# Kernel optimization log

Hardware: AMD Instinct MI355X
Metric: run time of the kernel (lower is better)

The kernel has to match this reference:

```python
import jax, jax.numpy as jnp
import numpy as np

EMBED_DIM = 1024
NUM_HEADS = 16
HEAD_DIM = EMBED_DIM // NUM_HEADS
B, T = 4, 2048


def quantum_layer(x):
    # Exact closed form of the RY + CNOT-chain + PauliZ circuit:
    # expval(Z_i) = prod_{j<=i} cos(x_j)  (cumulative product along feature dim)
    return jnp.cumprod(jnp.cos(x), axis=-1)


def separate_heads(x):
    b, s, _ = x.shape
    return x.reshape(b, s, NUM_HEADS, HEAD_DIM).transpose(0, 2, 1, 3)  # (B,H,T,D)


def combine_heads(x):
    b, h, s, d = x.shape
    return x.transpose(0, 2, 1, 3).reshape(b, s, h * d)


def setup_inputs() -> dict:
    key = jax.random.key(0)
    ks = jax.random.split(key, 9)
    scale = 1.0 / np.sqrt(EMBED_DIM)
    return {
        "x": jax.random.normal(ks[0], (B, T, EMBED_DIM), dtype=jnp.float32),
        "Wq": jax.random.normal(ks[1], (EMBED_DIM, EMBED_DIM), dtype=jnp.float32) * scale,
        "bq": jax.random.normal(ks[2], (EMBED_DIM,), dtype=jnp.float32) * 0.01,
        "Wk": jax.random.normal(ks[3], (EMBED_DIM, EMBED_DIM), dtype=jnp.float32) * scale,
        "bk": jax.random.normal(ks[4], (EMBED_DIM,), dtype=jnp.float32) * 0.01,
        "Wv": jax.random.normal(ks[5], (EMBED_DIM, EMBED_DIM), dtype=jnp.float32) * scale,
        "bv": jax.random.normal(ks[6], (EMBED_DIM,), dtype=jnp.float32) * 0.01,
        "Wo": jax.random.normal(ks[7], (EMBED_DIM, EMBED_DIM), dtype=jnp.float32) * scale,
        "bo": jax.random.normal(ks[8], (EMBED_DIM,), dtype=jnp.float32) * 0.01,
    }


def reference(x, Wq, bq, Wk, bk, Wv, bv, Wo, bo):
    k = x @ Wk + bk
    q = x @ Wq + bq
    v = x @ Wv + bv
    # quantum circuit applied to q and k projections
    q = quantum_layer(q)
    k = quantum_layer(k)
    # NOTE: source swaps roles: kqv = (heads(k), heads(q), heads(v)); q, h, v = kqv
    qh = separate_heads(k)   # acts as query
    kh = separate_heads(q)   # acts as key
    vh = separate_heads(v)
    scores = jnp.einsum("bhqd,bhkd->bhqk", qh, kh) / jnp.sqrt(jnp.float32(HEAD_DIM))
    attn = jax.nn.softmax(scores, axis=-1)  # dropout is identity in eval
    out = jnp.einsum("bhqk,bhkd->bhqd", attn, vh)
    return combine_heads(out) @ Wo + bo
```

## Files before the change

kernel.cpp:

```cpp
#include <hip/hip_runtime.h>
#include <hip/hip_bf16.h>

#define B_ 4
#define T_ 2048
#define E_ 1024
#define H_ 16
#define D_ 64
#define M_ (B_ * T_)

typedef unsigned short u16;
typedef unsigned int u32;
typedef short s16x8 __attribute__((ext_vector_type(8)));
typedef unsigned short u16x8 __attribute__((ext_vector_type(8)));
typedef float f32x4 __attribute__((ext_vector_type(4)));
typedef unsigned int u32x2 __attribute__((ext_vector_type(2)));

__device__ __forceinline__ u16 f2bf(float f) {
    __hip_bfloat16 h = __float2bfloat16(f);
    return __builtin_bit_cast(u16, h);
}
__device__ __forceinline__ float bf2f(u16 u) {
    unsigned int v = ((unsigned int)u) << 16;
    return __builtin_bit_cast(float, v);
}
__device__ __forceinline__ u32 pk2(float a, float b) {
    return (u32)f2bf(a) | ((u32)f2bf(b) << 16);
}

__device__ __forceinline__ int block_probe_is_bf16(const void* x, int tid) {
    const u16* p = (const u16*)x;
    u16 u = p[tid];
    int e = (u >> 7) & 0xFF;
    int ok = ((u & 0x7FFF) == 0 || (e >= 103 && e <= 133)) ? 1 : 0;
    return (__syncthreads_count(ok) >= 240) ? 1 : 0;
}

__global__ __launch_bounds__(256) void transpose_w_single_kernel(
    const void* __restrict__ w0, const void* __restrict__ w1,
    u16* __restrict__ o0, u16* __restrict__ o1,
    const void* __restrict__ xprobe)
{
    __shared__ u16 th[64][66];
    const int x = threadIdx.x, y = threadIdx.y;
    const int isbf = block_probe_is_bf16(xprobe, y * 64 + x);
    const void* in = blockIdx.z ? w1 : w0;
    u16* o = blockIdx.z ? o1 : o0;
    const int r0 = blockIdx.y * 64;
    const int c0 = blockIdx.x * 64;
    #pragma unroll
    for (int j = 0; j < 16; j++) {
        const size_t idx = (size_t)(r0 + y * 16 + j) * E_ + c0 + x;
        float v = isbf ? bf2f(((const u16*)in)[idx]) : ((const float*)in)[idx];
        th[y * 16 + j][x] = f2bf(v);
    }
    __syncthreads();
    #pragma unroll
    for (int j = 0; j < 16; j++)
        o[(size_t)(c0 + y * 16 + j) * E_ + r0 + x] = th[x][y * 16 + j];
}

__global__ __launch_bounds__(256) void convert_bias_kernel(
    const void* __restrict__ bq, const void* __restrict__ bk,
    const void* __restrict__ bv, const void* __restrict__ bo,
    float* __restrict__ outb, const void* __restrict__ xprobe)
{
    const int isbf = block_probe_is_bf16(xprobe, threadIdx.x);
    const int i = blockIdx.x * 256 + threadIdx.x;
    const int w = blockIdx.y;
    const void* p = (w == 0) ? bq : (w == 1) ? bk : (w == 2) ? bv : bo;
    float v = isbf ? bf2f(((const u16*)p)[i]) : ((const float*)p)[i];
    outb[w * 1024 + i] = v;
}

__global__ __launch_bounds__(256) void gemm_f32out_kernel(
    const void* __restrict__ A, int a_mode, int m_base,
    const u16* __restrict__ Bt, const float* __restrict__ bias,
    float* __restrict__ Cout, int ldc)
{
    __shared__ u16 a_lds[128 * 72];
    __shared__ u16 b_lds[128 * 72];
    const int tid = threadIdx.x;
    const int isbf = block_probe_is_bf16(A, tid);
    const int a_bf = (a_mode < 0) ? isbf : a_mode;
    const int wave = tid >> 6, lane = tid & 63;
    const int lane15 = lane & 15, quad = lane >> 4;
    const int wm = (wave & 1) * 64, wn = (wave >> 1) * 64;
    const int nwg = (int)(gridDim.x * gridDim.y);
    const int lin = (int)(blockIdx.y * gridDim.x + blockIdx.x);
    const int swz = (lin & 7) * (nwg >> 3) + (lin >> 3);
    const int m0 = (swz / (int)gridDim.x) * 128;
    const int n0 = (swz % (int)gridDim.x) * 128;
    const int srow = tid >> 1;
    const int soff = (tid & 1) * 32;

    f32x4 acc[4][4];
    #pragma unroll
    for (int i = 0; i < 4; i++)
        #pragma unroll
        for (int j = 0; j < 4; j++) acc[i][j] = (f32x4)0.0f;

    const u16* abase_bf = (const u16*)A + (size_t)(m_base + m0 + srow) * E_ + soff;
    const float* abase_f = (const float*)A + (size_t)(m_base + m0 + srow) * E_ + soff;
    const u16* bbase = Bt + (size_t)(n0 + srow) * E_ + soff;

    u16x8 av[4], bv[4];
    if (a_bf) {
        #pragma unroll
        for (int j = 0; j < 4; j++) av[j] = *(const u16x8*)(abase_bf + j * 8);
    } else {
        #pragma unroll
        for (int j = 0; j < 4; j++) {
            f32x4 t0 = *(const f32x4*)(abase_f + j * 8);
            f32x4 t1 = *(const f32x4*)(abase_f + j * 8 + 4);
            u16x8 o;
            #pragma unroll
            for (int e = 0; e < 4; e++) { o[e] = f2bf(t0[e]); o[4 + e] = f2bf(t1[e]); }
            av[j] = o;
        }
    }
    #pragma unroll
    for (int j = 0; j < 4; j++) bv[j] = *(const u16x8*)(bbase + j * 8);

    for (int kk = 0; kk < E_; kk += 64) {
        __syncthreads();
        #pragma unroll
        for (int j = 0; j < 4; j++) {
            *(u16x8*)&a_lds[srow * 72 + soff + j * 8] = av[j];
            *(u16x8*)&b_lds[srow * 72 + soff + j * 8] = bv[j];
        }
        __syncthreads();
        if (kk + 64 < E_) {
            const int k2 = kk + 64;
            if (a_bf) {
                #pragma unroll
                for (int j = 0; j < 4; j++) av[j] = *(const u16x8*)(abase_bf + k2 + j * 8);
            } else {
                #pragma unroll
                for (int j = 0; j < 4; j++) {
                    f32x4 t0 = *(const f32x4*)(abase_f + k2 + j * 8);
                    f32x4 t1 = *(const f32x4*)(abase_f + k2 + j * 8 + 4);
                    u16x8 o;
                    #pragma unroll
                    for (int e = 0; e < 4; e++) { o[e] = f2bf(t0[e]); o[4 + e] = f2bf(t1[e]); }
                    av[j] = o;
                }
            }
            #pragma unroll
            for (int j = 0; j < 4; j++) bv[j] = *(const u16x8*)(bbase + k2 + j * 8);
        }
        #pragma unroll
        for (int ks = 0; ks < 2; ks++) {
            s16x8 af[4], bfr[4];
            #pragma unroll
            for (int i = 0; i < 4; i++)
                af[i] = *(const s16x8*)&a_lds[(wm + i * 16 + lane15) * 72 + ks * 32 + quad * 8];
            #pragma unroll
            for (int j = 0; j < 4; j++)
                bfr[j] = *(const s16x8*)&b_lds[(wn + j * 16 + lane15) * 72 + ks * 32 + quad * 8];
            #pragma unroll
            for (int i = 0; i < 4; i++)
                #pragma unroll
                for (int j = 0; j < 4; j++)
                    acc[i][j] = __builtin_amdgcn_mfma_f32_16x16x32_bf16(af[i], bfr[j], acc[i][j], 0, 0, 0);
        }
    }

    #pragma unroll
    for (int j = 0; j < 4; j++) {
        const int col = n0 + wn + j * 16 + lane15;
        const float bb = bias[col];
        #pragma unroll
        for (int i = 0; i < 4; i++) {
            const int row = m0 + wm + i * 16 + quad * 4;
            #pragma unroll
            for (int r = 0; r < 4; r++)
                Cout[(size_t)(row + r) * ldc + col] = acc[i][j][r] + bb;
        }
    }
}

__global__ __launch_bounds__(256) void gemm_v_fused_kernel(
    const void* __restrict__ X, const u16* __restrict__ Bt,
    const float* __restrict__ bias, u16* __restrict__ Vt)
{
    __shared__ u16 smem[2 * 128 * 72];
    u16* a_lds = smem;
    u16* b_lds = smem + 128 * 72;
    const int tid = threadIdx.x;
    const int isbf = block_probe_is_bf16(X, tid);
    const int wave = tid >> 6, lane = tid & 63;
    const int lane15 = lane & 15, quad = lane >> 4;
    const int wm = (wave & 1) * 64, wn = (wave >> 1) * 64;
    const int nwg = (int)(gridDim.x * gridDim.y);
    const int lin = (int)(blockIdx.y * gridDim.x + blockIdx.x);
    const int swz = (lin & 7) * (nwg >> 3) + (lin >> 3);
    const int m0 = (swz / (int)gridDim.x) * 128;
    const int n0 = (swz % (int)gridDim.x) * 128;
    const int srow = tid >> 1;
    const int soff = (tid & 1) * 32;

    f32x4 acc[4][4];
    #pragma unroll
    for (int i = 0; i < 4; i++)
        #pragma unroll
        for (int j = 0; j < 4; j++) acc[i][j] = (f32x4)0.0f;

    const u16* abase_bf = (const u16*)X + (size_t)(m0 + srow) * E_ + soff;
    const float* abase_f = (const float*)X + (size_t)(m0 + srow) * E_ + soff;
    const u16* bbase = Bt + (size_t)(n0 + srow) * E_ + soff;

    u16x8 av[4], bv[4];
    if (isbf) {
        #pragma unroll
        for (int j = 0; j < 4; j++) av[j] = *(const u16x8*)(abase_bf + j * 8);
    } else {
        #pragma unroll
        for (int j = 0; j < 4; j++) {
            f32x4 t0 = *(const f32x4*)(abase_f + j * 8);
            f32x4 t1 = *(const f32x4*)(abase_f + j * 8 + 4);
            u16x8 o;
            #pragma unroll
            for (int e = 0; e < 4; e++) { o[e] = f2bf(t0[e]); o[4 + e] = f2bf(t1[e]); }
            av[j] = o;
        }
    }
    #pragma unroll
    for (int j = 0; j < 4; j++) bv[j] = *(const u16x8*)(bbase + j * 8);

    for (int kk = 0; kk < E_; kk += 64) {
        __syncthreads();
        #pragma unroll
        for (int j = 0; j < 4; j++) {
            *(u16x8*)&a_lds[srow * 72 + soff + j * 8] = av[j];
            *(u16x8*)&b_lds[srow * 72 + soff + j * 8] = bv[j];
        }
        __syncthreads();
        if (kk + 64 < E_) {
            const int k2 = kk + 64;
            if (isbf) {
                #pragma unroll
                for (int j = 0; j < 4; j++) av[j] = *(const u16x8*)(abase_bf + k2 + j * 8);
            } else {
                #pragma unroll
                for (int j = 0; j < 4; j++) {
                    f32x4 t0 = *(const f32x4*)(abase_f + k2 + j * 8);
                    f32x4 t1 = *(const f32x4*)(abase_f + k2 + j * 8 + 4);
                    u16x8 o;
                    #pragma unroll
                    for (int e = 0; e < 4; e++) { o[e] = f2bf(t0[e]); o[4 + e] = f2bf(t1[e]); }
                    av[j] = o;
                }
            }
            #pragma unroll
            for (int j = 0; j < 4; j++) bv[j] = *(const u16x8*)(bbase + k2 + j * 8);
        }
        #pragma unroll
        for (int ks = 0; ks < 2; ks++) {
            s16x8 af[4], bfr[4];
            #pragma unroll
            for (int i = 0; i < 4; i++)
                af[i] = *(const s16x8*)&a_lds[(wm + i * 16 + lane15) * 72 + ks * 32 + quad * 8];
            #pragma unroll
            for (int j = 0; j < 4; j++)
                bfr[j] = *(const s16x8*)&b_lds[(wn + j * 16 + lane15) * 72 + ks * 32 + quad * 8];
            #pragma unroll
            for (int i = 0; i < 4; i++)
                #pragma unroll
                for (int j = 0; j < 4; j++)
                    acc[i][j] = __builtin_amdgcn_mfma_f32_16x16x32_bf16(af[i], bfr[j], acc[i][j], 0, 0, 0);
        }
    }

    __syncthreads();
    u16* c_tile = smem;
    #pragma unroll
    for (int j = 0; j < 4; j++) {
        const float bb = bias[n0 + wn + j * 16 + lane15];
        #pragma unroll
        for (int i = 0; i < 4; i++)
            #pragma unroll
            for (int r = 0; r < 4; r++)
                c_tile[(wm + i * 16 + quad * 4 + r) * 132 + wn + j * 16 + lane15] =
                    f2bf(acc[i][j][r] + bb);
    }
    __syncthreads();
    const int b = m0 >> 11, t0 = m0 & 2047;
    const int orow = tid >> 1, half = tid & 1;
    u16* dst = Vt + ((size_t)b * 1024 + n0 + orow) * T_ + t0 + half * 64;
    #pragma unroll
    for (int c = 0; c < 8; c++) {
        u16x8 o;
        #pragma unroll
        for (int e = 0; e < 8; e++)
            o[e] = c_tile[(half * 64 + c * 8 + e) * 132 + orow];
        *(u16x8*)(dst + c * 8) = o;
    }
}

__global__ __launch_bounds__(256) void quantum2_kernel(
    const float* __restrict__ in, u16* __restrict__ key, u16* __restrict__ qry)
{
    const int wave = threadIdx.x >> 6, lane = threadIdx.x & 63;
    const int unit = (int)blockIdx.x * 4 + wave;
    const int row = unit >> 1, seg = unit & 1;
    const float* p = in + (size_t)row * 2048 + seg * 1024 + lane * 16;
    float v[16];
    #pragma unroll
    for (int j = 0; j < 16; j += 4) {
        f32x4 t = *(const f32x4*)(p + j);
        v[j] = t[0]; v[j + 1] = t[1]; v[j + 2] = t[2]; v[j + 3] = t[3];
    }
    float pl[16];
    float run = 1.0f;
    #pragma unroll
    for (int j = 0; j < 16; j++) { run *= cosf(v[j]); pl[j] = run; }
    float incl = run;
    #pragma unroll
    for (int off = 1; off < 64; off <<= 1) {
        float t = __shfl_up(incl, off);
        if (lane >= off) incl *= t;
    }
    float pref = __shfl_up(incl, 1);
    if (lane == 0) pref = 1.0f;
    u16x8 o0, o1;
    #pragma unroll
    for (int j = 0; j < 8; j++) {
        o0[j] = f2bf(pref * pl[j]);
        o1[j] = f2bf(pref * pl[j + 8]);
    }
    u16* outp = (seg ? qry : key) + (size_t)row * E_ + lane * 16;
    *(u16x8*)(outp) = o0;
    *(u16x8*)(outp + 8) = o1;
}

__global__ __launch_bounds__(256, 4) void attn_kernel(
    const u16* __restrict__ Qrm, const u16* __restrict__ Krm,
    const u16* __restrict__ Vt, u16* __restrict__ Orm)
{
    __shared__ u16 k_lds[64 * 72];
    __shared__ u16 v_lds[64 * 72];
    __shared__ u16 p_lds[128 * 72];
    const int tid = threadIdx.x;
    const int wave = tid >> 6, lane = tid & 63;
    const int lane15 = lane & 15, quad = lane >> 4;

    const int lin = (int)(blockIdx.x + gridDim.x * blockIdx.y);
    const int swz = (lin & 7) * 128 + (lin >> 3);
    const int t0 = (swz & 15) * 128;
    const int bh = swz >> 4;
    const int b = bh >> 4, h = bh & 15;

    s16x8 qf[2][2];
    #pragma unroll
    for (int mt = 0; mt < 2; mt++)
        #pragma unroll
        for (int ks = 0; ks < 2; ks++) {
            const u16* src = Qrm
                + (size_t)(b * T_ + t0 + wave * 32 + mt * 16 + lane15) * E_
                + h * 64 + ks * 32 + quad * 8;
            u16x8 t = *(const u16x8*)src;
            u16x8 o;
            #pragma unroll
            for (int e = 0; e < 8; e++) o[e] = f2bf(bf2f(t[e]) * 0.125f);
            qf[mt][ks] = __builtin_bit_cast(s16x8, o);
        }

    f32x4 lsum4[2];
    f32x4 oacc[2][4];
    #pragma unroll
    for (int mt = 0; mt < 2; mt++) {
        lsum4[mt] = (f32x4)0.0f;
        #pragma unroll
        for (int n = 0; n < 4; n++) oacc[mt][n] = (f32x4)0.0f;
    }

    const u16* kbase = Krm + (size_t)(b * T_) * E_ + h * 64;
    const u16* vbase = Vt + (size_t)bh * 64 * T_;
    const int srow = tid >> 2;
    const int soff = (tid & 3) * 16;

    u16x8 kpre0, kpre1, vpre0, vpre1;
    {
        const u16* ksrc = kbase + (size_t)srow * E_ + soff;
        kpre0 = *(const u16x8*)(ksrc);
        kpre1 = *(const u16x8*)(ksrc + 8);
        const u16* vsrc = vbase + (size_t)srow * T_ + soff;
        vpre0 = *(const u16x8*)(vsrc);
        vpre1 = *(const u16x8*)(vsrc + 8);
    }

    for (int tk0 = 0; tk0 < T_; tk0 += 64) {
        __syncthreads();
        *(u16x8*)&k_lds[srow * 72 + soff]     = kpre0;
        *(u16x8*)&k_lds[srow * 72 + soff + 8] = kpre1;
        *(u16x8*)&v_lds[srow * 72 + soff]     = vpre0;
        *(u16x8*)&v_lds[srow * 72 + soff + 8] = vpre1;
        __syncthreads();

        if (tk0 + 64 < T_) {
            const u16* ksrc = kbase + (size_t)(tk0 + 64 + srow) * E_ + soff;
            kpre0 = *(const u16x8*)(ksrc);
            kpre1 = *(const u16x8*)(ksrc + 8);
            const u16* vsrc = vbase + (size_t)srow * T_ + tk0 + 64 + soff;
            vpre0 = *(const u16x8*)(vsrc);
            vpre1 = *(const u16x8*)(vsrc + 8);
        }

        f32x4 sacc[2][4];
        #pragma unroll
        for (int mt = 0; mt < 2; mt++)
            #pragma unroll
            for (int j = 0; j < 4; j++) sacc[mt][j] = (f32x4)0.0f;
        #pragma unroll
        for (int ks = 0; ks < 2; ks++) {
            s16x8 kb[4];
            #pragma unroll
            for (int j = 0; j < 4; j++)
                kb[j] = *(const s16x8*)&k_lds[(j * 16 + lane15) * 72 + ks * 32 + quad * 8];
            #pragma unroll
            for (int mt = 0; mt < 2; mt++)
                #pragma unroll
                for (int j = 0; j < 4; j++)
                    sacc[mt][j] = __builtin_amdgcn_mfma_f32_16x16x32_bf16(
                        kb[j], qf[mt][ks], sacc[mt][j], 0, 0, 0);
        }

        #pragma unroll
        for (int mt = 0; mt < 2; mt++)
            #pragma unroll
            for (int j = 0; j < 4; j++) {
                const f32x4 s = sacc[mt][j];
                const float p0 = __expf(s[0]);
                const float p1 = __expf(s[1]);
                const float p2 = __expf(s[2]);
                const float p3 = __expf(s[3]);
                lsum4[mt][0] += p0; lsum4[mt][1] += p1;
                lsum4[mt][2] += p2; lsum4[mt][3] += p3;
                u32x2 w;
                w[0] = pk2(p0, p1);
                w[1] = pk2(p2, p3);
                *(u32x2*)&p_lds[(wave * 32 + mt * 16 + lane15) * 72 + j * 16 + quad * 4] = w;
            }

        #pragma unroll
        for (int ks = 0; ks < 2; ks++) {
            s16x8 pa[2], vb[4];
            #pragma unroll
            for (int mt = 0; mt < 2; mt++)
                pa[mt] = *(const s16x8*)&p_lds[(wave * 32 + mt * 16 + lane15) * 72 + ks * 32 + quad * 8];
            #pragma unroll
            for (int n = 0; n < 4; n++)
                vb[n] = *(const s16x8*)&v_lds[(n * 16 + lane15) * 72 + ks * 32 + quad * 8];
            #pragma unroll
            for (int mt = 0; mt < 2; mt++)
                #pragma unroll
                for (int n = 0; n < 4; n++)
                    oacc[mt][n] = __builtin_amdgcn_mfma_f32_16x16x32_bf16(
                        pa[mt], vb[n], oacc[mt][n], 0, 0, 0);
        }
    }

    #pragma unroll
    for (int mt = 0; mt < 2; mt++) {
        float l = lsum4[mt][0] + lsum4[mt][1] + lsum4[mt][2] + lsum4[mt][3];
        l += __shfl_xor(l, 16);
        l += __shfl_xor(l, 32);
        #pragma unroll
        for (int r = 0; r < 4; r++) {
            const float lr = __shfl(l, quad * 4 + r);
            const float inv = 1.0f / lr;
            const size_t row = (size_t)(b * T_ + t0 + wave * 32 + mt * 16 + quad * 4 + r);
            #pragma unroll
            for (int n = 0; n < 4; n++)
                Orm[row * E_ + h * 64 + n * 16 + lane15] = f2bf(oacc[mt][n][r] * inv);
        }
    }
}

extern "C" void kernel_launch(void* const* d_in, const int* in_sizes, int n_in,
                              void* d_out, int out_size, void* d_ws, size_t ws_size,
                              hipStream_t stream) {
    (void)in_sizes; (void)n_in; (void)out_size; (void)ws_size;
    const void* x  = d_in[0];
    const void* Wq = d_in[1];
    const void* bq = d_in[2];
    const void* Wk = d_in[3];
    const void* bk = d_in[4];
    const void* Wv = d_in[5];
    const void* bv = d_in[6];
    const void* Wo = d_in[7];
    const void* bo = d_in[8];

    char* ws = (char*)d_ws;
    const size_t MB = 1024 * 1024;
    u16*   wt_o  = (u16*)(ws);
    float* biasf = (float*)(ws + 2 * MB);
    u16*   wt_qk = (u16*)(ws + 3 * MB);
    u16*   wt_v  = (u16*)(ws + 7 * MB);
    u16*   key   = (u16*)(ws + 9 * MB);
    u16*   qry   = (u16*)(ws + 25 * MB);
    float* tmp   = (float*)(ws + 41 * MB);
    u16*   vt    = (u16*)(ws + 41 * MB);
    u16*   orm   = (u16*)(ws + 57 * MB);

    transpose_w_single_kernel<<<dim3(16, 16, 2), dim3(64, 4), 0, stream>>>(
        Wq, Wk, wt_qk, wt_qk + 1024 * 1024, x);
    transpose_w_single_kernel<<<dim3(16, 16, 2), dim3(64, 4), 0, stream>>>(
        Wv, Wo, wt_v, wt_o, x);
    convert_bias_kernel<<<dim3(4, 4), 256, 0, stream>>>(
        bq, bk, bv, bo, biasf, x);

    for (int hh = 0; hh < 2; hh++) {
        gemm_f32out_kernel<<<dim3(16, 32), 256, 0, stream>>>(
            x, -1, hh * 4096, wt_qk, biasf, tmp, 2048);
        quantum2_kernel<<<2048, 256, 0, stream>>>(
            tmp, key + (size_t)hh * 4096 * E_, qry + (size_t)hh * 4096 * E_);
    }

    gemm_v_fused_kernel<<<dim3(8, 64), 256, 0, stream>>>(x, wt_v, biasf + 2 * 1024, vt);

    attn_kernel<<<dim3(16, 64), 256, 0, stream>>>(qry, key, vt, orm);

    gemm_f32out_kernel<<<dim3(8, 64), 256, 0, stream>>>(
        orm, 1, 0, wt_o, biasf + 3 * 1024, (float*)d_out, 1024);
}
```

Measured before the change: 456.5 us.

## Load GEMM tiles directly into LDS with global_load_lds, drop register prefetch

The GEMM kernel now loads bf16 A and B tiles straight from global memory into LDS using the direct-to-LDS load builtin, replacing the register-staged prefetch, and the padded LDS row stride goes from 72 to 64. This cuts VGPR pressure and removes the register-to-LDS copy, but it also drops the software overlap of the next tile's loads with the current tile's MFMAs. The unpadded stride may cause LDS bank conflicts on fragment reads. The attention kernel's minimum-blocks launch bound is also removed.

```diff
diff --git a/kernel.cpp b/kernel.cpp
--- a/kernel.cpp
+++ b/kernel.cpp
@@ -1,5 +1,6 @@
 #include <hip/hip_runtime.h>
 #include <hip/hip_bf16.h>
+#include <stdint.h>
 
 #define B_ 4
 #define T_ 2048
@@ -25,6 +26,15 @@
 }
 __device__ __forceinline__ u32 pk2(float a, float b) {
     return (u32)f2bf(a) | ((u32)f2bf(b) << 16);
+}
+
+typedef __attribute__((address_space(1))) const void as1_void;
+typedef __attribute__((address_space(3))) void as3_void;
+__device__ __forceinline__ void gload16(const void* g, void* l) {
+    __builtin_amdgcn_global_load_lds(
+        reinterpret_cast<as1_void*>(reinterpret_cast<uintptr_t>(g)),
+        reinterpret_cast<as3_void*>(reinterpret_cast<uintptr_t>(l)),
+        16, 0, 0);
 }
 
 __device__ __forceinline__ int block_probe_is_bf16(const void* x, int tid) {
@@ -77,8 +87,8 @@
     const u16* __restrict__ Bt, const float* __restrict__ bias,
     float* __restrict__ Cout, int ldc)
 {
-    __shared__ u16 a_lds[128 * 72];
-    __shared__ u16 b_lds[128 * 72];
+    __shared__ u16 a_lds[128 * 64];
+    __shared__ u16 b_lds[128 * 64];
     const int tid = threadIdx.x;
     const int isbf = block_probe_is_bf16(A, tid);
     const int a_bf = (a_mode < 0) ? isbf : a_mode;
@@ -90,73 +100,52 @@
     const int swz = (lin & 7) * (nwg >> 3) + (lin >> 3);
     const int m0 = (swz / (int)gridDim.x) * 128;
     const int n0 = (swz % (int)gridDim.x) * 128;
+
+    f32x4 acc[4][4];
+    #pragma unroll
+    for (int i = 0; i < 4; i++)
+        #pragma unroll
+        for (int j = 0; j < 4; j++) acc[i][j] = (f32x4)0.0f;
+
+    const int g_r = wave * 32 + (lane >> 3);
+    const int g_c = (lane & 7) * 8;
+    const u16* ga = (const u16*)A + (size_t)(m_base + m0 + g_r) * E_ + g_c;
+    const u16* gb = Bt + (size_t)(n0 + g_r) * E_ + g_c;
     const int srow = tid >> 1;
     const int soff = (tid & 1) * 32;
-
-    f32x4 acc[4][4];
-    #pragma unroll
-    for (int i = 0; i < 4; i++)
-        #pragma unroll
-        for (int j = 0; j < 4; j++) acc[i][j] = (f32x4)0.0f;
-
-    const u16* abase_bf = (const u16*)A + (size_t)(m_base + m0 + srow) * E_ + soff;
     const float* abase_f = (const float*)A + (size_t)(m_base + m0 + srow) * E_ + soff;
-    const u16* bbase = Bt + (size_t)(n0 + srow) * E_ + soff;
-
-    u16x8 av[4], bv[4];
-    if (a_bf) {
-        #pragma unroll
-        for (int j = 0; j < 4; j++) av[j] = *(const u16x8*)(abase_bf + j * 8);
-    } else {
-        #pragma unroll
-        for (int j = 0; j < 4; j++) {
-            f32x4 t0 = *(const f32x4*)(abase_f + j * 8);
-            f32x4 t1 = *(const f32x4*)(abase_f + j * 8 + 4);
-            u16x8 o;
-            #pragma unroll
-            for (int e = 0; e < 4; e++) { o[e] = f2bf(t0[e]); o[4 + e] = f2bf(t1[e]); }
-            av[j] = o;
-        }
-    }
-    #pragma unroll
-    for (int j = 0; j < 4; j++) bv[j] = *(const u16x8*)(bbase + j * 8);
 
     for (int kk = 0; kk < E_; kk += 64) {
         __syncthreads();
-        #pragma unroll
-        for (int j = 0; j < 4; j++) {
-            *(u16x8*)&a_lds[srow * 72 + soff + j * 8] = av[j];
-            *(u16x8*)&b_lds[srow * 72 + soff + j * 8] = bv[j];
-        }
+        if (a_bf) {
+            #pragma unroll
+            for (int j = 0; j < 4; j++)
+                gload16(ga + (size_t)j * 8 * E_ + kk, &a_lds[(wave * 4 + j) * 512]);
+        } else {
+            #pragma unroll
+            for (int j = 0; j < 4; j++) {
+                f32x4 t0 = *(const f32x4*)(abase_f + kk + j * 8);
+                f32x4 t1 = *(const f32x4*)(abase_f + kk + j * 8 + 4);
+                u16x8 o;
+                #pragma unroll
+                for (int e = 0; e < 4; e++) { o[e] = f2bf(t0[e]); o[4 + e] = f2bf(t1[e]); }
+                *(u16x8*)&a_lds[srow * 64 + soff + j * 8] = o;
+            }
+        }
+        #pragma unroll
+        for (int j = 0; j < 4; j++)
+            gload16(gb + (size_t)j * 8 * E_ + kk, &b_lds[(wave * 4 + j) * 512]);
         __syncthreads();
-        if (kk + 64 < E_) {
-            const int k2 = kk + 64;
-            if (a_bf) {
-                #pragma unroll
-                for (int j = 0; j < 4; j++) av[j] = *(const u16x8*)(abase_bf + k2 + j * 8);
-            } else {
-                #pragma unroll
-                for (int j = 0; j < 4; j++) {
-                    f32x4 t0 = *(const f32x4*)(abase_f + k2 + j * 8);
-                    f32x4 t1 = *(const f32x4*)(abase_f + k2 + j * 8 + 4);
-                    u16x8 o;
-                    #pragma unroll
-                    for (int e = 0; e < 4; e++) { o[e] = f2bf(t0[e]); o[4 + e] = f2bf(t1[e]); }
-                    av[j] = o;
-                }
-            }
-            #pragma unroll
-            for (int j = 0; j < 4; j++) bv[j] = *(const u16x8*)(bbase + k2 + j * 8);
-        }
+
         #pragma unroll
         for (int ks = 0; ks < 2; ks++) {
             s16x8 af[4], bfr[4];
             #pragma unroll
             for (int i = 0; i < 4; i++)
-                af[i] = *(const s16x8*)&a_lds[(wm + i * 16 + lane15) * 72 + ks * 32 + quad * 8];
+                af[i] = *(const s16x8*)&a_lds[(wm + i * 16 + lane15) * 64 + ks * 32 + quad * 8];
             #pragma unroll
             for (int j = 0; j < 4; j++)
-                bfr[j] = *(const s16x8*)&b_lds[(wn + j * 16 + lane15) * 72 + ks * 32 + quad * 8];
+                bfr[j] = *(const s16x8*)&b_lds[(wn + j * 16 + lane15) * 64 + ks * 32 + quad * 8];
             #pragma unroll
             for (int i = 0; i < 4; i++)
                 #pragma unroll
@@ -333,7 +322,7 @@
     *(u16x8*)(outp + 8) = o1;
 }
 
-__global__ __launch_bounds__(256, 4) void attn_kernel(
+__global__ __launch_bounds__(256) void attn_kernel(
     const u16* __restrict__ Qrm, const u16* __restrict__ Krm,
     const u16* __restrict__ Vt, u16* __restrict__ Orm)
 {
```

Measured after the change: 419.4 us. 8.1% less time.
